# Kernel tuning notes

Measured on AMD Instinct MI355X. Metric: run time of the kernel, lower is better.

## Reference

```python
import jax, jax.numpy as jnp
import numpy as np

B, T = 1024, 128
T_IN, A_IN, V_IN = 300, 74, 35
D = 128            # dim_capsule
H = D // 2
ROUTING = 3
LABEL = 1


def _glorot(key, shape):
    fan_out, fan_in = shape[-2], shape[-1]
    s = jnp.sqrt(2.0 / (fan_in + fan_out)).astype(jnp.float32)
    return jax.random.normal(key, shape, jnp.float32) * s


def setup_inputs() -> dict:
    k = iter(jax.random.split(jax.random.key(0), 40))
    inp = {}
    inp["text"] = jax.random.normal(next(k), (B, T, T_IN), jnp.float32)
    inp["audio"] = jax.random.normal(next(k), (B, T, A_IN), jnp.float32)
    inp["video"] = jax.random.normal(next(k), (B, T, V_IN), jnp.float32)
    # bidirectional encoder LSTMs (hidden = D//2 per direction); biases b = b_ih + b_hh
    for p, din in (("t", T_IN), ("a", A_IN), ("v", V_IN)):
        for d in ("f", "b"):
            inp[p + "_Wih_" + d] = _glorot(next(k), (4 * H, din))
            inp[p + "_Whh_" + d] = _glorot(next(k), (4 * H, H))
            inp[p + "_b_" + d] = jnp.zeros((4 * H,), jnp.float32)
    # 4 capsule projection matrices per modality, stacked [4, D, D]
    inp["Wt"] = _glorot(next(k), (4, D, D))
    inp["Wa"] = _glorot(next(k), (4, D, D))
    inp["Wv"] = _glorot(next(k), (4, D, D))
    # routing LSTMs (ta, tv, av, tav) stacked on leading axis
    inp["r_Wih"] = _glorot(next(k), (4, 4 * D, D))
    inp["r_Whh"] = _glorot(next(k), (4, 4 * D, D))
    inp["r_b"] = jnp.zeros((4, 4 * D), jnp.float32)
    # decision bidirectional LSTM (hidden = D per direction)
    for d in ("f", "b"):
        inp["d_Wih_" + d] = _glorot(next(k), (4 * D, D))
        inp["d_Whh_" + d] = _glorot(next(k), (4 * D, D))
        inp["d_b_" + d] = jnp.zeros((4 * D,), jnp.float32)
    inp["fc1_W"] = _glorot(next(k), (H, D))
    inp["fc1_b"] = jnp.zeros((H,), jnp.float32)
    inp["fc2_W"] = _glorot(next(k), (LABEL, H))
    inp["fc2_b"] = jnp.zeros((LABEL,), jnp.float32)
    inp["batch_size"] = B
    return inp


def _lstm_final(x, Wih, Whh, b):
    # x: [B, T, I] -> final hidden state [B, Hh]; torch gate order i, f, g, o
    Hh = Whh.shape[-1]
    z = jnp.zeros((x.shape[0], Hh), x.dtype)

    def step(carry, xt):
        h, c = carry
        g = xt @ Wih.T + h @ Whh.T + b
        i, f, gg, o = jnp.split(g, 4, axis=-1)
        c = jax.nn.sigmoid(f) * c + jax.nn.sigmoid(i) * jnp.tanh(gg)
        h = jax.nn.sigmoid(o) * jnp.tanh(c)
        return (h, c), None

    (h, _), _ = jax.lax.scan(step, (z, z), jnp.swapaxes(x, 0, 1))
    return h


def _forward(text, audio, video,
             t_Wih_f, t_Whh_f, t_b_f, t_Wih_b, t_Whh_b, t_b_b,
             a_Wih_f, a_Whh_f, a_b_f, a_Wih_b, a_Whh_b, a_b_b,
             v_Wih_f, v_Whh_f, v_b_f, v_Wih_b, v_Whh_b, v_b_b,
             Wt, Wa, Wv, r_Wih, r_Whh, r_b,
             d_Wih_f, d_Whh_f, d_b_f, d_Wih_b, d_Whh_b, d_b_b,
             fc1_W, fc1_b, fc2_W, fc2_b):
    Bsz = text.shape[0]

    def ctx(x, Wf, Uf, bf, Wb, Ub, bb):
        # biLSTM final hidden, fwd||bwd concat -> [B, 1, D]
        hf = _lstm_final(x, Wf, Uf, bf)
        hb = _lstm_final(x[:, ::-1], Wb, Ub, bb)
        return jnp.concatenate([hf, hb], -1)[:, None, :]

    tc = ctx(text, t_Wih_f, t_Whh_f, t_b_f, t_Wih_b, t_Whh_b, t_b_b)
    ac = ctx(audio, a_Wih_f, a_Whh_f, a_b_f, a_Wih_b, a_Whh_b, a_b_b)
    vc = ctx(video, v_Wih_f, v_Whh_f, v_b_f, v_Wih_b, v_Whh_b, v_b_b)

    tusc = jnp.einsum('bod,kde->kboe', tc, Wt)   # [4, B, 1, D]
    ausc = jnp.einsum('bod,kde->kboe', ac, Wa)
    vusc = jnp.einsum('bod,kde->kboe', vc, Wv)

    pre = [jnp.concatenate([tusc[0], ausc[0]], 1),                # ta  [B,2,D]
           jnp.concatenate([tusc[1], vusc[0]], 1),                # tv  [B,2,D]
           jnp.concatenate([ausc[1], vusc[1]], 1),                # av  [B,2,D]
           jnp.concatenate([tusc[2], ausc[2], vusc[2]], 1)]       # tav [B,3,D]

    rc = [jnp.ones((Bsz, n, D), text.dtype) for n in (2, 2, 2, 3, 7)]
    dc = None
    for r in range(ROUTING + 1):
        rc = [jax.nn.softmax(c, axis=1) for c in rc]
        # per-pair routing LSTMs, final hidden [B,1,D]
        bc = [_lstm_final(rc[i] * pre[i], r_Wih[i], r_Whh[i], r_b[i])[:, None, :]
              for i in range(4)]
        deci = jnp.concatenate([tusc[3], ausc[3], vusc[3]] + bc, 1)  # [B,7,D]
        xd = rc[4] * deci
        # decision biLSTM: sum of both directions' final hidden -> [B,1,D]
        dc = (_lstm_final(xd, d_Wih_f, d_Whh_f, d_b_f)
              + _lstm_final(xd[:, ::-1], d_Wih_b, d_Whh_b, d_b_b))[:, None, :]
        if r < ROUTING:
            # agreement update: bmm gives [B,n,1], broadcasts over last dim (== repeat)
            rc = [rc[i] + jnp.matmul(pre[i], jnp.swapaxes(bc[i], 1, 2)) for i in range(4)] \
                 + [rc[4] + jnp.matmul(deci, jnp.swapaxes(dc, 1, 2))]

    dc = dc[:, 0, :]
    o1 = jnp.tanh(dc @ fc1_W.T + fc1_b)
    return o1 @ fc2_W.T + fc2_b   # mosi: no output tanh


def reference(text, audio, video,
              t_Wih_f, t_Whh_f, t_b_f, t_Wih_b, t_Whh_b, t_b_b,
              a_Wih_f, a_Whh_f, a_b_f, a_Wih_b, a_Whh_b, a_b_b,
              v_Wih_f, v_Whh_f, v_b_f, v_Wih_b, v_Whh_b, v_b_b,
              Wt, Wa, Wv, r_Wih, r_Whh, r_b,
              d_Wih_f, d_Whh_f, d_b_f, d_Wih_b, d_Whh_b, d_b_b,
              fc1_W, fc1_b, fc2_W, fc2_b, batch_size):
    return _forward(text, audio, video,
                    t_Wih_f, t_Whh_f, t_b_f, t_Wih_b, t_Whh_b, t_b_b,
                    a_Wih_f, a_Whh_f, a_b_f, a_Wih_b, a_Whh_b, a_b_b,
                    v_Wih_f, v_Whh_f, v_b_f, v_Wih_b, v_Whh_b, v_b_b,
                    Wt, Wa, Wv, r_Wih, r_Whh, r_b,
                    d_Wih_f, d_Whh_f, d_b_f, d_Wih_b, d_Whh_b, d_b_b,
                    fc1_W, fc1_b, fc2_W, fc2_b)
```

## Files before the change

kernel.cpp:

```cpp
#include <hip/hip_runtime.h>

typedef __bf16 bf16;
typedef _Float16 f16;
typedef f16 f16x8 __attribute__((ext_vector_type(8)));
typedef float f32x4 __attribute__((ext_vector_type(4)));

__device__ __forceinline__ f32x4 mfma16h(f16x8 a, f16x8 b, f32x4 c) {
  return __builtin_amdgcn_mfma_f32_16x16x32_f16(a, b, c, 0, 0, 0);
}
__device__ __forceinline__ float sigm(float x) { return 1.0f / (1.0f + __expf(-x)); }
__device__ __forceinline__ float tanh_f(float x) {
  float e = __expf(-2.0f * fabsf(x));
  return copysignf((1.0f - e) / (1.0f + e), x);
}
__device__ __forceinline__ float ldin(const void* p, long i, int f32m) {
  if (f32m) return ((const float*)p)[i];
  unsigned u = (unsigned)((const unsigned short*)p)[i] << 16;
  return __uint_as_float(u);
}
__device__ __forceinline__ unsigned short f16u(f16 h) { return __builtin_bit_cast(unsigned short, h); }
__device__ __forceinline__ float bfc(unsigned short s) { return __uint_as_float((unsigned)s << 16); }

__global__ void detect_dtype(const unsigned short* __restrict__ p, int* __restrict__ flag) {
  __shared__ int cnt;
  if (threadIdx.x == 0) cnt = 0;
  __syncthreads();
  int c = 0;
  for (int i = threadIdx.x; i < 4096; i += 256) {
    unsigned e = (p[2 * i] >> 7) & 0xFFu;
    if (e >= 0xC0u) ++c;
  }
  atomicAdd(&cnt, c);
  __syncthreads();
  if (threadIdx.x == 0) *flag = (cnt > 64) ? 1 : 0;
}


struct PadArgs { const void* src[6]; };
struct HiloArgs { const void* src[12]; int n[12]; int off[12]; };
struct F32Args { const void* src[16]; int n[16]; int off[16]; };

__global__ void conv_all(PadArgs pa, HiloArgs ha, F32Args fa,
                         f16* __restrict__ wo, float* __restrict__ fm,
                         const int* __restrict__ flag) {
  const int y = blockIdx.y;
  const int f32m = *flag;
  if (y < 6) {
    const int dinT[6] = {300, 300, 74, 74, 35, 35};
    const int kpT[6] = {320, 320, 96, 96, 64, 64};
    const int offT[6] = {0, 81920, 163840, 188416, 212992, 229376};
    int din = dinT[y], kp = kpT[y];
    const void* s = pa.src[y];
    f16* o = wo + offT[y];
    int total = 256 * kp;
    for (int i = blockIdx.x * blockDim.x + threadIdx.x; i < total; i += gridDim.x * blockDim.x) {
      int n = i / kp, k = i - n * kp;
      float v = (k < din) ? ldin(s, n * din + k, f32m) : 0.0f;
      o[i] = (f16)v;
    }
  } else if (y < 18) {
    int j = y - 6;
    int n = ha.n[j];
    const void* s = ha.src[j];
    f16* o = wo + ha.off[j];
    for (int i = blockIdx.x * blockDim.x + threadIdx.x; i < n; i += gridDim.x * blockDim.x)
      o[i] = (f16)ldin(s, i, f32m);
  } else {
    int j = y - 18;
    int n = fa.n[j];
    const void* s = fa.src[j];
    float* d = fm + fa.off[j];
    for (int i = blockIdx.x * blockDim.x + threadIdx.x; i < n; i += gridDim.x * blockDim.x)
      d[i] = ldin(s, i, f32m);
  }
}

__global__ void init_rc(float* __restrict__ rcs) {
  int i = blockIdx.x * 256 + threadIdx.x;
  if (i < 16384) rcs[i] = 1.0f;
}

struct TriArgs {
  const void* x[3];
  const f16* wAll;
  const float* fmisc;
  float* ctx;
  const int* flag;
};

template <int DIN, int KP, int CHUNK, int F32M>
__device__ void tri_body(const void* __restrict__ xsrc,
                         const f16* __restrict__ wp, const f16* __restrict__ whh,
                         const float* __restrict__ bias, float* __restrict__ ctx,
                         int m, int d, int b0, char* sm) {
  constexpr int XP = KP + 8;
  constexpr int NKS = KP / 32;
  constexpr int NCH = DIN / CHUNK;
  constexpr int ITER = (NCH + 15) / 16;

  f16 (*Xhi)[XP] = (f16 (*)[XP])sm;
  f16 (*Xlo)[XP] = (f16 (*)[XP])(sm + 32 * XP * 2);
  f16 (*hbuf)[16][72] = (f16 (*)[16][72])(sm + 64 * XP * 2);
  float* gbuf = (float*)(sm + 64 * XP * 2 + 4608);

  const int tid = threadIdx.x;
  const int lane = tid & 63, n16 = lane & 15, q = lane >> 4, w8 = tid >> 6;
  const int srow = tid & 31, sct = tid >> 5;
  const int hc = tid & 63, rr = tid >> 6;

  f16x8 wihr[2][NKS];
  f16x8 whr[2][2];
#pragma unroll
  for (int t = 0; t < 2; ++t) {
    int cc = (w8 + t * 8) * 16 + n16;
#pragma unroll
    for (int ks = 0; ks < NKS; ++ks)
      wihr[t][ks] = *(const f16x8*)(wp + cc * KP + ks * 32 + q * 8);
#pragma unroll
    for (int ks = 0; ks < 2; ++ks)
      whr[t][ks] = *(const f16x8*)(whh + cc * 64 + ks * 32 + q * 8);
  }
  float bgm[4];
#pragma unroll
  for (int g = 0; g < 4; ++g) bgm[g] = bias[g * 64 + hc];

  {
    unsigned* z = (unsigned*)sm;
    int nz = (64 * XP * 2 + 4608) >> 2;
    for (int i = tid; i < nz; i += 512) z[i] = 0u;
  }

  uint4 pf[ITER];
  auto stage_load = [&](int tg) {
#pragma unroll
    for (int i = 0; i < ITER; ++i) {
      int c = sct + i * 16;
      if (c < NCH) {
        int tl = srow >> 4, bb = srow & 15;
        int t = tg * 2 + tl; if (d) t = 127 - t;
        long base = ((long)(b0 + bb) * 128 + t) * DIN + c * CHUNK;
        if (F32M) {
          const float* p = (const float*)xsrc + base;
          if constexpr (CHUNK == 4) pf[i] = *(const uint4*)p;
          else if constexpr (CHUNK == 2) { uint2 v = *(const uint2*)p; pf[i].x = v.x; pf[i].y = v.y; }
          else pf[i].x = *(const unsigned*)p;
        } else {
          const unsigned short* p = (const unsigned short*)xsrc + base;
          if constexpr (CHUNK == 4) { uint2 v = *(const uint2*)p; pf[i].x = v.x; pf[i].y = v.y; }
          else if constexpr (CHUNK == 2) pf[i].x = *(const unsigned*)p;
          else pf[i].x = *p;
        }
      }
    }
  };
  auto stage_store = [&]() {
#pragma unroll
    for (int i = 0; i < ITER; ++i) {
      int c = sct + i * 16;
      if (c < NCH) {
        float v[4];
        if (F32M) {
          v[0] = __uint_as_float(pf[i].x); v[1] = __uint_as_float(pf[i].y);
          v[2] = __uint_as_float(pf[i].z); v[3] = __uint_as_float(pf[i].w);
        } else {
          v[0] = bfc((unsigned short)(pf[i].x & 0xFFFF));
          v[1] = bfc((unsigned short)(pf[i].x >> 16));
          v[2] = bfc((unsigned short)(pf[i].y & 0xFFFF));
          v[3] = bfc((unsigned short)(pf[i].y >> 16));
        }
        unsigned short hb[4], lb[4];
#pragma unroll
        for (int e = 0; e < CHUNK; ++e) {
          f16 h = (f16)v[e];
          hb[e] = f16u(h);
          lb[e] = f16u((f16)(v[e] - (float)h));
        }
        if constexpr (CHUNK == 4) {
          uint2 H; H.x = hb[0] | ((unsigned)hb[1] << 16); H.y = hb[2] | ((unsigned)hb[3] << 16);
          *(uint2*)&Xhi[srow][c * 4] = H;
          if (F32M) {
            uint2 L; L.x = lb[0] | ((unsigned)lb[1] << 16); L.y = lb[2] | ((unsigned)lb[3] << 16);
            *(uint2*)&Xlo[srow][c * 4] = L;
          }
        } else if constexpr (CHUNK == 2) {
          *(unsigned*)&Xhi[srow][c * 2] = hb[0] | ((unsigned)hb[1] << 16);
          if (F32M) *(unsigned*)&Xlo[srow][c * 2] = lb[0] | ((unsigned)lb[1] << 16);
        } else {
          *(unsigned short*)&Xhi[srow][c] = hb[0];
          if (F32M) *(unsigned short*)&Xlo[srow][c] = lb[0];
        }
      }
    }
  };

  float c2[2] = {0.f, 0.f};
  stage_load(0);
  __syncthreads();

  for (int tg = 0; tg < 64; ++tg) {
    stage_store();
    if (tg < 63) stage_load(tg + 1);
    __syncthreads();

    f32x4 a00, a01, a10, a11;
    {
      const f32x4 zf = {0.f, 0.f, 0.f, 0.f};
      a00 = zf; a01 = zf; a10 = zf; a11 = zf;
    }
#pragma unroll
    for (int ks = 0; ks < NKS; ++ks) {
      f16x8 ah0 = *(const f16x8*)(&Xhi[n16][ks * 32 + q * 8]);
      f16x8 ah1 = *(const f16x8*)(&Xhi[16 + n16][ks * 32 + q * 8]);
      a00 = mfma16h(ah0, wihr[0][ks], a00);
      a01 = mfma16h(ah0, wihr[1][ks], a01);
      a10 = mfma16h(ah1, wihr[0][ks], a10);
      a11 = mfma16h(ah1, wihr[1][ks], a11);
      if (F32M) {
        f16x8 al0 = *(const f16x8*)(&Xlo[n16][ks * 32 + q * 8]);
        f16x8 al1 = *(const f16x8*)(&Xlo[16 + n16][ks * 32 + q * 8]);
        a00 = mfma16h(al0, wihr[0][ks], a00);
        a01 = mfma16h(al0, wihr[1][ks], a01);
        a10 = mfma16h(al1, wihr[0][ks], a10);
        a11 = mfma16h(al1, wihr[1][ks], a11);
      }
    }

    {
      f16x8 h0 = *(const f16x8*)(&hbuf[0][n16][q * 8]);
      f16x8 h1 = *(const f16x8*)(&hbuf[0][n16][32 + q * 8]);
      a00 = mfma16h(h0, whr[0][0], a00); a00 = mfma16h(h1, whr[0][1], a00);
      a01 = mfma16h(h0, whr[1][0], a01); a01 = mfma16h(h1, whr[1][1], a01);
    }
#pragma unroll
    for (int e = 0; e < 4; ++e) {
      gbuf[(q * 4 + e) * 260 + w8 * 16 + n16] = a00[e];
      gbuf[(q * 4 + e) * 260 + 128 + w8 * 16 + n16] = a01[e];
    }
    __syncthreads();

#pragma unroll
    for (int e = 0; e < 2; ++e) {
      int row = rr + e * 8;
      float gi = gbuf[row * 260 + hc] + bgm[0];
      float gf = gbuf[row * 260 + 64 + hc] + bgm[1];
      float gg = gbuf[row * 260 + 128 + hc] + bgm[2];
      float go = gbuf[row * 260 + 192 + hc] + bgm[3];
      float c = sigm(gf) * c2[e] + sigm(gi) * tanh_f(gg);
      c2[e] = c;
      float h = sigm(go) * tanh_f(c);
      hbuf[1][row][hc] = (f16)h;
    }
    __syncthreads();

    {
      f16x8 h0 = *(const f16x8*)(&hbuf[1][n16][q * 8]);
      f16x8 h1 = *(const f16x8*)(&hbuf[1][n16][32 + q * 8]);
      a10 = mfma16h(h0, whr[0][0], a10); a10 = mfma16h(h1, whr[0][1], a10);
      a11 = mfma16h(h0, whr[1][0], a11); a11 = mfma16h(h1, whr[1][1], a11);
    }
#pragma unroll
    for (int e = 0; e < 4; ++e) {
      gbuf[(q * 4 + e) * 260 + w8 * 16 + n16] = a10[e];
      gbuf[(q * 4 + e) * 260 + 128 + w8 * 16 + n16] = a11[e];
    }
    __syncthreads();

    const bool lastStep = (tg == 63);
#pragma unroll
    for (int e = 0; e < 2; ++e) {
      int row = rr + e * 8;
      float gi = gbuf[row * 260 + hc] + bgm[0];
      float gf = gbuf[row * 260 + 64 + hc] + bgm[1];
      float gg = gbuf[row * 260 + 128 + hc] + bgm[2];
      float go = gbuf[row * 260 + 192 + hc] + bgm[3];
      float c = sigm(gf) * c2[e] + sigm(gi) * tanh_f(gg);
      c2[e] = c;
      float h = sigm(go) * tanh_f(c);
      hbuf[0][row][hc] = (f16)h;
      if (lastStep) ctx[(m * 1024 + b0 + row) * 128 + d * 64 + hc] = h;
    }
  }
}

__global__ __launch_bounds__(512, 2) void tri_lstm(TriArgs A) {
  __shared__ __align__(16) char sm[64 * 328 * 2 + 4608 + 16640];
  int bid = blockIdx.x;
  int md = bid >> 6, xb = bid & 63;
  int m = md >> 1, d = md & 1, b0 = xb * 16;
  const int wpOffT[6] = {0, 81920, 163840, 188416, 212992, 229376};
  const f16* wp = A.wAll + wpOffT[md];
  const f16* whh = A.wAll + 245760 + md * 16384;
  const float* bias = A.fmisc + md * 256;
  int f32m = *A.flag;
  if (f32m) {
    if (m == 0)      tri_body<300, 320, 4, 1>(A.x[0], wp, whh, bias, A.ctx, m, d, b0, sm);
    else if (m == 1) tri_body<74, 96, 2, 1>(A.x[1], wp, whh, bias, A.ctx, m, d, b0, sm);
    else             tri_body<35, 64, 1, 1>(A.x[2], wp, whh, bias, A.ctx, m, d, b0, sm);
  } else {
    if (m == 0)      tri_body<300, 320, 4, 0>(A.x[0], wp, whh, bias, A.ctx, m, d, b0, sm);
    else if (m == 1) tri_body<74, 96, 2, 0>(A.x[1], wp, whh, bias, A.ctx, m, d, b0, sm);
    else             tri_body<35, 64, 1, 0>(A.x[2], wp, whh, bias, A.ctx, m, d, b0, sm);
  }
}

__global__ __launch_bounds__(128) void usc_kern(const float* __restrict__ ctx,
                                                const float* __restrict__ fmisc,
                                                float* __restrict__ usc) {
  __shared__ float cr[4][128];
  int b0 = blockIdx.x * 4;
  int mk = blockIdx.y, mod = mk >> 2;
  int e = threadIdx.x;
  const float* W = fmisc + 4608 + mk * 16384;
  for (int i = e; i < 512; i += 128) {
    int r = i >> 7, dd = i & 127;
    cr[r][dd] = ctx[(mod * 1024 + b0 + r) * 128 + dd];
  }
  __syncthreads();
  float a0 = 0.f, a1 = 0.f, a2 = 0.f, a3 = 0.f;
  for (int dd = 0; dd < 128; ++dd) {
    float wv = W[dd * 128 + e];
    a0 += cr[0][dd] * wv; a1 += cr[1][dd] * wv;
    a2 += cr[2][dd] * wv; a3 += cr[3][dd] * wv;
  }
  usc[(mk * 1024 + b0 + 0) * 128 + e] = a0;
  usc[(mk * 1024 + b0 + 1) * 128 + e] = a1;
  usc[(mk * 1024 + b0 + 2) * 128 + e] = a2;
  usc[(mk * 1024 + b0 + 3) * 128 + e] = a3;
}

#define LSTM_STEP_DECL \
  const int tid = threadIdx.x; \
  const int lane = tid & 63, n16 = lane & 15, q = lane >> 4, w = tid >> 6; \
  const int u = w * 16 + n16; \
  const int u2 = tid & 127, rgg = tid >> 7;

__device__ __forceinline__ void lstm_step_mfma_r(
    f32x4* acc, const f16 (*xh)[16][136], const f16 (*xl)[16][136],
    const f16 (*hh)[16][136], int p,
    const f16x8 (*bhf)[4], const f16x8 (*whf)[4],
    int n16, int q) {
#pragma unroll
  for (int ks = 0; ks < 4; ++ks) {
    f16x8 axh = *(const f16x8*)(&xh[p][n16][ks * 32 + q * 8]);
    f16x8 axl = *(const f16x8*)(&xl[p][n16][ks * 32 + q * 8]);
    f16x8 ahh = *(const f16x8*)(&hh[p][n16][ks * 32 + q * 8]);
#pragma unroll
    for (int g = 0; g < 4; ++g) {
      acc[g] = mfma16h(axh, bhf[g][ks], acc[g]);
      acc[g] = mfma16h(axl, bhf[g][ks], acc[g]);
      acc[g] = mfma16h(ahh, whf[g][ks], acc[g]);
    }
  }
}

__global__ __launch_bounds__(512) void rchain(const float* __restrict__ usc,
                                              const float* __restrict__ rcs,
                                              const f16* __restrict__ wAll,
                                              const float* __restrict__ fmisc,
                                              float* __restrict__ bcg) {
  __shared__ __align__(16) f16 xh[2][16][136], xl[2][16][136], hh[2][16][136];
  __shared__ float rcl[16][3];
  LSTM_STEP_DECL
  const int chain = blockIdx.y;
  const int b0 = blockIdx.x * 16;
  const int WihOff[4] = {344064, 409600, 475136, 540672};
  const int WhhOff[4] = {606208, 671744, 737280, 802816};
  const int bOff[4] = {1536, 2048, 2560, 3072};
  const int ns = (chain == 3) ? 3 : 2;

  if (tid < 16) {
    int row = tid;
    int goff = (chain == 3) ? 6 : chain * 2;
    float v[3], mx = -1e30f;
    for (int j = 0; j < ns; ++j) { v[j] = rcs[(b0 + row) * 16 + goff + j]; mx = fmaxf(mx, v[j]); }
    float s = 0.f;
    for (int j = 0; j < ns; ++j) { v[j] = __expf(v[j] - mx); s += v[j]; }
    float inv = 1.0f / s;
    for (int j = 0; j < ns; ++j) rcl[row][j] = v[j] * inv;
  }
  for (int i = tid; i < 2 * 16 * 136; i += 512) (&hh[0][0][0])[i] = (f16)0.0f;

  const f16* Whh = wAll + WhhOff[chain];
  const f16* Wih = wAll + WihOff[chain];
  f16x8 whf[4][4], bhf[4][4];
#pragma unroll
  for (int g = 0; g < 4; ++g)
#pragma unroll
    for (int ks = 0; ks < 4; ++ks) {
      whf[g][ks] = *(const f16x8*)(Whh + (g * 128 + u) * 128 + ks * 32 + q * 8);
      bhf[g][ks] = *(const f16x8*)(Wih + (g * 128 + u) * 128 + ks * 32 + q * 8);
    }
  const float* bias = fmisc + bOff[chain];
  float bg[4];
#pragma unroll
  for (int g = 0; g < 4; ++g) bg[g] = bias[g * 128 + u];

  const int preMk0[4] = {0, 1, 5, 2};
  const int preMk1[4] = {4, 8, 9, 6};
  float creg[4] = {0.f, 0.f, 0.f, 0.f};

  float pv[4];
  {
    int mk0 = preMk0[chain];
#pragma unroll
    for (int rr = 0; rr < 4; ++rr)
      pv[rr] = usc[(mk0 * 1024 + b0 + rgg * 4 + rr) * 128 + u2];
  }
  __syncthreads();

  for (int s = 0; s < ns; ++s) {
    int p = s & 1;
#pragma unroll
    for (int rr = 0; rr < 4; ++rr) {
      int row = rgg * 4 + rr;
      float xv = rcl[row][s] * pv[rr];
      f16 xhv = (f16)xv;
      xh[p][row][u2] = xhv;
      xl[p][row][u2] = (f16)(xv - (float)xhv);
    }
    if (s + 1 < ns) {
      int mk2 = (s + 1 == 1) ? preMk1[chain] : 10;
#pragma unroll
      for (int rr = 0; rr < 4; ++rr)
        pv[rr] = usc[(mk2 * 1024 + b0 + rgg * 4 + rr) * 128 + u2];
    }
    __syncthreads();
    f32x4 acc[4];
    const f32x4 zf = {0.f, 0.f, 0.f, 0.f};
#pragma unroll
    for (int g = 0; g < 4; ++g) acc[g] = zf;
    lstm_step_mfma_r(acc, xh, xl, hh, p, bhf, whf, n16, q);
#pragma unroll
    for (int e = 0; e < 4; ++e) {
      int row = q * 4 + e;
      float gi = acc[0][e] + bg[0];
      float gf = acc[1][e] + bg[1];
      float gg = acc[2][e] + bg[2];
      float go = acc[3][e] + bg[3];
      float c = sigm(gf) * creg[e] + sigm(gi) * tanh_f(gg);
      creg[e] = c;
      float h = sigm(go) * tanh_f(c);
      hh[p ^ 1][row][u] = (f16)h;
      if (s == ns - 1) bcg[(chain * 1024 + b0 + row) * 128 + u] = h;
    }
  }
}

__global__ __launch_bounds__(512) void decision(const float* __restrict__ usc,
                                                const float* __restrict__ rcs,
                                                const f16* __restrict__ wAll,
                                                const float* __restrict__ fmisc,
                                                const float* __restrict__ bcg,
                                                float* __restrict__ dcF,
                                                float* __restrict__ dcB) {
  __shared__ __align__(16) f16 xh[2][16][136], xl[2][16][136], hh[2][16][136];
  __shared__ float rcl[16][7];
  LSTM_STEP_DECL
  const int dir = blockIdx.y;
  const int b0 = blockIdx.x * 16;

  if (tid < 16) {
    int row = tid;
    float v[7], mx = -1e30f;
    for (int j = 0; j < 7; ++j) { v[j] = rcs[(b0 + row) * 16 + 9 + j]; mx = fmaxf(mx, v[j]); }
    float s = 0.f;
    for (int j = 0; j < 7; ++j) { v[j] = __expf(v[j] - mx); s += v[j]; }
    float inv = 1.0f / s;
    for (int j = 0; j < 7; ++j) rcl[row][j] = v[j] * inv;
  }
  for (int i = tid; i < 2 * 16 * 136; i += 512) (&hh[0][0][0])[i] = (f16)0.0f;

  const int WihOffD[2] = {868352, 999424};
  const int WhhOffD[2] = {933888, 1064960};
  const int bOffD[2] = {3584, 4096};
  const f16* Whh = wAll + WhhOffD[dir];
  const f16* Wih = wAll + WihOffD[dir];
  f16x8 whf[4][4], bhf[4][4];
#pragma unroll
  for (int g = 0; g < 4; ++g)
#pragma unroll
    for (int ks = 0; ks < 4; ++ks) {
      whf[g][ks] = *(const f16x8*)(Whh + (g * 128 + u) * 128 + ks * 32 + q * 8);
      bhf[g][ks] = *(const f16x8*)(Wih + (g * 128 + u) * 128 + ks * 32 + q * 8);
    }
  const float* bias = fmisc + bOffD[dir];
  float bg[4];
#pragma unroll
  for (int g = 0; g < 4; ++g) bg[g] = bias[g * 128 + u];

  const int dmk[3] = {3, 7, 11};
  float creg[4] = {0.f, 0.f, 0.f, 0.f};

  float pv[4];
  {
    int j0 = dir ? 6 : 0;
#pragma unroll
    for (int rr = 0; rr < 4; ++rr) {
      int row = rgg * 4 + rr;
      pv[rr] = (j0 < 3) ? usc[(dmk[j0] * 1024 + b0 + row) * 128 + u2]
                        : bcg[((j0 - 3) * 1024 + b0 + row) * 128 + u2];
    }
  }
  __syncthreads();

  for (int s = 0; s < 7; ++s) {
    int p = s & 1;
    int j = dir ? (6 - s) : s;
#pragma unroll
    for (int rr = 0; rr < 4; ++rr) {
      int row = rgg * 4 + rr;
      float xv = rcl[row][j] * pv[rr];
      f16 xhv = (f16)xv;
      xh[p][row][u2] = xhv;
      xl[p][row][u2] = (f16)(xv - (float)xhv);
    }
    if (s < 6) {
      int j2 = dir ? (5 - s) : (s + 1);
#pragma unroll
      for (int rr = 0; rr < 4; ++rr) {
        int row = rgg * 4 + rr;
        pv[rr] = (j2 < 3) ? usc[(dmk[j2] * 1024 + b0 + row) * 128 + u2]
                          : bcg[((j2 - 3) * 1024 + b0 + row) * 128 + u2];
      }
    }
    __syncthreads();
    f32x4 acc[4];
    const f32x4 zf = {0.f, 0.f, 0.f, 0.f};
#pragma unroll
    for (int g = 0; g < 4; ++g) acc[g] = zf;
    lstm_step_mfma_r(acc, xh, xl, hh, p, bhf, whf, n16, q);
#pragma unroll
    for (int e = 0; e < 4; ++e) {
      int row = q * 4 + e;
      float gi = acc[0][e] + bg[0];
      float gf = acc[1][e] + bg[1];
      float gg = acc[2][e] + bg[2];
      float go = acc[3][e] + bg[3];
      float c = sigm(gf) * creg[e] + sigm(gi) * tanh_f(gg);
      creg[e] = c;
      float h = sigm(go) * tanh_f(c);
      hh[p ^ 1][row][u] = (f16)h;
      if (s == 6) {
        if (dir == 0) dcF[(b0 + row) * 128 + u] = h;
        else dcB[(b0 + row) * 128 + u] = h;
      }
    }
  }
}

__global__ __launch_bounds__(256) void rupdate(const float* __restrict__ usc,
                                               const float* __restrict__ bcg,
                                               const float* __restrict__ dcF,
                                               const float* __restrict__ dcB,
                                               float* __restrict__ rcs,
                                               float* __restrict__ dcw, int last) {
  __shared__ float dsum[16][128];
  __shared__ float rcl[16][16];
  const int tid = threadIdx.x;
  const int b0 = blockIdx.x * 16;
  for (int i = tid; i < 2048; i += 256) {
    int row = i >> 7, col = i & 127;
    float v = dcF[(b0 + row) * 128 + col] + dcB[(b0 + row) * 128 + col];
    dsum[row][col] = v;
    if (last) dcw[(b0 + row) * 128 + col] = v;
  }
  {
    int row = tid >> 4, cap = tid & 15;
    rcl[row][cap] = rcs[(b0 + row) * 16 + cap];
  }
  __syncthreads();
  if (!last) {
    int row = tid >> 4, cap = tid & 15;
    const int goffT[16] = {0, 0, 2, 2, 4, 4, 6, 6, 6, 9, 9, 9, 9, 9, 9, 9};
    const int gnT[16] = {2, 2, 2, 2, 2, 2, 3, 3, 3, 7, 7, 7, 7, 7, 7, 7};
    int go = goffT[cap], gn = gnT[cap];
    float mx = -1e30f;
    for (int j = 0; j < gn; ++j) mx = fmaxf(mx, rcl[row][go + j]);
    float s = 0.f;
    for (int j = 0; j < gn; ++j) s += __expf(rcl[row][go + j] - mx);
    float sm = __expf(rcl[row][cap] - mx) / s;

    const int preMkTab[9] = {0, 4, 1, 8, 5, 9, 2, 6, 10};
    float a = 0.f;
    if (cap < 9) {
      int i = (cap < 6) ? (cap >> 1) : 3;
      const float* pr = usc + (preMkTab[cap] * 1024 + b0 + row) * 128;
      const float* bcrow = bcg + (i * 1024 + b0 + row) * 128;
      for (int dd = 0; dd < 128; ++dd) a += pr[dd] * bcrow[dd];
    } else {
      int j = cap - 9;
      if (j < 3) {
        const int dmk[3] = {3, 7, 11};
        const float* pr = usc + (dmk[j] * 1024 + b0 + row) * 128;
        for (int dd = 0; dd < 128; ++dd) a += pr[dd] * dsum[row][dd];
      } else {
        const float* bcrow = bcg + ((j - 3) * 1024 + b0 + row) * 128;
        for (int dd = 0; dd < 128; ++dd) a += bcrow[dd] * dsum[row][dd];
      }
    }
    rcs[(b0 + row) * 16 + cap] = sm + a;
  }
}

__global__ __launch_bounds__(64) void head(const float* __restrict__ dc, const float* __restrict__ fcw,
                                           void* __restrict__ out, const int* __restrict__ flag) {
  int b = blockIdx.x, j = threadIdx.x;
  const float* r = dc + b * 128;
  float acc = fcw[209408 + j];
  for (int dd = 0; dd < 128; ++dd) acc += r[dd] * fcw[201216 + j * 128 + dd];
  float o = tanh_f(acc) * fcw[209472 + j];
  for (int off = 32; off; off >>= 1) o += __shfl_down(o, off, 64);
  if (j == 0) {
    float res = o + fcw[209536];
    if (*flag) ((float*)out)[b] = res;
    else ((bf16*)out)[b] = (bf16)res;
  }
}

extern "C" void kernel_launch(void* const* d_in, const int* in_sizes, int n_in,
                              void* d_out, int out_size, void* d_ws, size_t ws_size,
                              hipStream_t stream) {
  float* fw = (float*)d_ws;
  int* flag = (int*)d_ws;
  float* ctx = fw + 4;
  float* usc = ctx + 393216;
  float* dcw = usc + 1572864;
  float* fmisc = dcw + 131072;
  float* rcs = fmisc + 209552;
  float* bcg = rcs + 16384;
  float* dcF = bcg + 524288;
  float* dcB = dcF + 131072;
  f16* wAll = (f16*)(dcB + 131072);

  hipLaunchKernelGGL(detect_dtype, dim3(1), dim3(256), 0, stream,
                     (const unsigned short*)d_in[0], flag);

  PadArgs pa;
  HiloArgs ha;
  for (int m = 0; m < 3; ++m)
    for (int dd = 0; dd < 2; ++dd) {
      int md = m * 6 + dd * 3;
      pa.src[m * 2 + dd] = d_in[3 + md + 0];
      ha.src[m * 2 + dd] = d_in[3 + md + 1];
      ha.n[m * 2 + dd] = 16384;
      ha.off[m * 2 + dd] = 245760 + (m * 2 + dd) * 16384;
    }
  const int hsrc[6] = {24, 25, 27, 28, 30, 31};
  const int hn[6] = {262144, 262144, 65536, 65536, 65536, 65536};
  const int hoff[6] = {344064, 606208, 868352, 933888, 999424, 1064960};
  for (int j = 0; j < 6; ++j) { ha.src[6 + j] = d_in[hsrc[j]]; ha.n[6 + j] = hn[j]; ha.off[6 + j] = hoff[j]; }

  F32Args fa;
  for (int m = 0; m < 3; ++m)
    for (int dd = 0; dd < 2; ++dd) {
      fa.src[m * 2 + dd] = d_in[3 + m * 6 + dd * 3 + 2];
      fa.n[m * 2 + dd] = 256;
      fa.off[m * 2 + dd] = (m * 2 + dd) * 256;
    }
  const int fsrc[10] = {26, 29, 32, 21, 22, 23, 33, 34, 35, 36};
  const int fn[10] = {2048, 512, 512, 65536, 65536, 65536, 8192, 64, 64, 1};
  const int foff[10] = {1536, 3584, 4096, 4608, 70144, 135680, 201216, 209408, 209472, 209536};
  for (int j = 0; j < 10; ++j) { fa.src[6 + j] = d_in[fsrc[j]]; fa.n[6 + j] = fn[j]; fa.off[6 + j] = foff[j]; }

  hipLaunchKernelGGL(conv_all, dim3(64, 34), dim3(256), 0, stream,
                     pa, ha, fa, wAll, fmisc, (const int*)flag);
  hipLaunchKernelGGL(init_rc, dim3(64), dim3(256), 0, stream, rcs);

  TriArgs ta;
  ta.x[0] = d_in[0]; ta.x[1] = d_in[1]; ta.x[2] = d_in[2];
  ta.wAll = wAll; ta.fmisc = fmisc; ta.ctx = ctx; ta.flag = flag;
  hipLaunchKernelGGL(tri_lstm, dim3(384), dim3(512), 0, stream, ta);

  hipLaunchKernelGGL(usc_kern, dim3(256, 12), dim3(128), 0, stream,
                     (const float*)ctx, (const float*)fmisc, usc);

  for (int r = 0; r < 4; ++r) {
    hipLaunchKernelGGL(rchain, dim3(64, 4), dim3(512), 0, stream,
                       (const float*)usc, (const float*)rcs, (const f16*)wAll,
                       (const float*)fmisc, bcg);
    hipLaunchKernelGGL(decision, dim3(64, 2), dim3(512), 0, stream,
                       (const float*)usc, (const float*)rcs, (const f16*)wAll,
                       (const float*)fmisc, (const float*)bcg, dcF, dcB);
    hipLaunchKernelGGL(rupdate, dim3(64), dim3(256), 0, stream,
                       (const float*)usc, (const float*)bcg, (const float*)dcF,
                       (const float*)dcB, rcs, dcw, (r == 3) ? 1 : 0);
  }

  hipLaunchKernelGGL(head, dim3(1024), dim3(64), 0, stream,
                     (const float*)dcw, (const float*)fmisc, d_out, (const int*)flag);
}
```

Measured before the change: 803.6 us.

## Fuse routing-coefficient update into rchain/decision prologues and double-buffer state

```diff
diff --git a/kernel.cpp b/kernel.cpp
--- a/kernel.cpp
+++ b/kernel.cpp
@@ -34,7 +34,6 @@
   __syncthreads();
   if (threadIdx.x == 0) *flag = (cnt > 64) ? 1 : 0;
 }
-
 
 struct PadArgs { const void* src[6]; };
 struct HiloArgs { const void* src[12]; int n[12]; int off[12]; };
@@ -73,11 +72,6 @@
     for (int i = blockIdx.x * blockDim.x + threadIdx.x; i < n; i += gridDim.x * blockDim.x)
       d[i] = ldin(s, i, f32m);
   }
-}
-
-__global__ void init_rc(float* __restrict__ rcs) {
-  int i = blockIdx.x * 256 + threadIdx.x;
-  if (i < 16384) rcs[i] = 1.0f;
 }
 
 struct TriArgs {
@@ -334,6 +328,49 @@
   const int u = w * 16 + n16; \
   const int u2 = tid & 127, rgg = tid >> 7;
 
+#define RCS_PROLOGUE(ROWS, DEST) \
+  if (tid < (ROWS) * 16) { \
+    int prow = tid >> 4, cap = tid & 15; \
+    float v = 1.0f; \
+    if (r > 0) { \
+      const int goffT[16] = {0, 0, 2, 2, 4, 4, 6, 6, 6, 9, 9, 9, 9, 9, 9, 9}; \
+      const int gnT[16] = {2, 2, 2, 2, 2, 2, 3, 3, 3, 7, 7, 7, 7, 7, 7, 7}; \
+      const int preMkTab[9] = {0, 4, 1, 8, 5, 9, 2, 6, 10}; \
+      const int dmkT[3] = {3, 7, 11}; \
+      int gn = gnT[cap]; \
+      float smv; \
+      if (r == 1) smv = 1.0f / (float)gn; \
+      else { \
+        int go = goffT[cap]; \
+        float mx = -1e30f; \
+        for (int j2 = 0; j2 < gn; ++j2) mx = fmaxf(mx, rcsIn[(b0 + prow) * 16 + go + j2]); \
+        float ssum = 0.f; \
+        for (int j2 = 0; j2 < gn; ++j2) ssum += __expf(rcsIn[(b0 + prow) * 16 + go + j2] - mx); \
+        smv = __expf(rcsIn[(b0 + prow) * 16 + cap] - mx) / ssum; \
+      } \
+      float a = 0.f; \
+      if (cap < 9) { \
+        int ii = (cap < 6) ? (cap >> 1) : 3; \
+        const float* pr = usc + (preMkTab[cap] * 1024 + b0 + prow) * 128; \
+        const float* bcrow = bcgPrev + (ii * 1024 + b0 + prow) * 128; \
+        for (int dd = 0; dd < 128; ++dd) a += pr[dd] * bcrow[dd]; \
+      } else { \
+        int j2 = cap - 9; \
+        const float* df = dcFprev + (b0 + prow) * 128; \
+        const float* db2 = dcBprev + (b0 + prow) * 128; \
+        if (j2 < 3) { \
+          const float* pr = usc + (dmkT[j2] * 1024 + b0 + prow) * 128; \
+          for (int dd = 0; dd < 128; ++dd) a += pr[dd] * (df[dd] + db2[dd]); \
+        } else { \
+          const float* bcrow = bcgPrev + ((j2 - 3) * 1024 + b0 + prow) * 128; \
+          for (int dd = 0; dd < 128; ++dd) a += bcrow[dd] * (df[dd] + db2[dd]); \
+        } \
+      } \
+      v = smv + a; \
+    } \
+    (DEST)[prow][cap] = v; \
+  }
+
 __device__ __forceinline__ void lstm_step_mfma_r(
     f32x4* acc, const f16 (*xh)[16][136], const f16 (*xl)[16][136],
     const f16 (*hh)[16][136], int p,
@@ -354,11 +391,17 @@
 }
 
 __global__ __launch_bounds__(512) void rchain(const float* __restrict__ usc,
-                                              const float* __restrict__ rcs,
+                                              const float* __restrict__ rcsIn,
+                                              float* __restrict__ rcsOut,
                                               const f16* __restrict__ wAll,
                                               const float* __restrict__ fmisc,
-                                              float* __restrict__ bcg) {
+                                              const float* __restrict__ bcgPrev,
+                                              const float* __restrict__ dcFprev,
+                                              const float* __restrict__ dcBprev,
+                                              float* __restrict__ bcg,
+                                              int r) {
   __shared__ __align__(16) f16 xh[2][16][136], xl[2][16][136], hh[2][16][136];
+  __shared__ float rr16[16][16];
   __shared__ float rcl[16][3];
   LSTM_STEP_DECL
   const int chain = blockIdx.y;
@@ -368,17 +411,21 @@
   const int bOff[4] = {1536, 2048, 2560, 3072};
   const int ns = (chain == 3) ? 3 : 2;
 
+  RCS_PROLOGUE(16, rr16)
+  for (int i = tid; i < 2 * 16 * 136; i += 512) (&hh[0][0][0])[i] = (f16)0.0f;
+  __syncthreads();
   if (tid < 16) {
     int row = tid;
     int goff = (chain == 3) ? 6 : chain * 2;
     float v[3], mx = -1e30f;
-    for (int j = 0; j < ns; ++j) { v[j] = rcs[(b0 + row) * 16 + goff + j]; mx = fmaxf(mx, v[j]); }
+    for (int j = 0; j < ns; ++j) { v[j] = rr16[row][goff + j]; mx = fmaxf(mx, v[j]); }
     float s = 0.f;
     for (int j = 0; j < ns; ++j) { v[j] = __expf(v[j] - mx); s += v[j]; }
     float inv = 1.0f / s;
     for (int j = 0; j < ns; ++j) rcl[row][j] = v[j] * inv;
   }
-  for (int i = tid; i < 2 * 16 * 136; i += 512) (&hh[0][0][0])[i] = (f16)0.0f;
+  if (chain == 0 && (r == 1 || r == 2) && tid < 256)
+    rcsOut[(b0 + (tid >> 4)) * 16 + (tid & 15)] = rr16[tid >> 4][tid & 15];
 
   const f16* Whh = wAll + WhhOff[chain];
   const f16* Wih = wAll + WihOff[chain];
@@ -403,17 +450,17 @@
   {
     int mk0 = preMk0[chain];
 #pragma unroll
-    for (int rr = 0; rr < 4; ++rr)
-      pv[rr] = usc[(mk0 * 1024 + b0 + rgg * 4 + rr) * 128 + u2];
+    for (int rr2 = 0; rr2 < 4; ++rr2)
+      pv[rr2] = usc[(mk0 * 1024 + b0 + rgg * 4 + rr2) * 128 + u2];
   }
   __syncthreads();
 
   for (int s = 0; s < ns; ++s) {
     int p = s & 1;
 #pragma unroll
-    for (int rr = 0; rr < 4; ++rr) {
-      int row = rgg * 4 + rr;
-      float xv = rcl[row][s] * pv[rr];
+    for (int rr2 = 0; rr2 < 4; ++rr2) {
+      int row = rgg * 4 + rr2;
+      float xv = rcl[row][s] * pv[rr2];
       f16 xhv = (f16)xv;
       xh[p][row][u2] = xhv;
       xl[p][row][u2] = (f16)(xv - (float)xhv);
@@ -421,8 +468,8 @@
     if (s + 1 < ns) {
       int mk2 = (s + 1 == 1) ? preMk1[chain] : 10;
 #pragma unroll
-      for (int rr = 0; rr < 4; ++rr)
-        pv[rr] = usc[(mk2 * 1024 + b0 + rgg * 4 + rr) * 128 + u2];
+      for (int rr2 = 0; rr2 < 4; ++rr2)
+        pv[rr2] = usc[(mk2 * 1024 + b0 + rgg * 4 + rr2) * 128 + u2];
     }
     __syncthreads();
     f32x4 acc[4];
@@ -447,28 +494,39 @@
 }
 
 __global__ __launch_bounds__(512) void decision(const float* __restrict__ usc,
-                                                const float* __restrict__ rcs,
+                                                const float* __restrict__ rcsIn,
                                                 const f16* __restrict__ wAll,
                                                 const float* __restrict__ fmisc,
+                                                const float* __restrict__ bcgPrev,
+                                                const float* __restrict__ dcFprev,
+                                                const float* __restrict__ dcBprev,
                                                 const float* __restrict__ bcg,
                                                 float* __restrict__ dcF,
-                                                float* __restrict__ dcB) {
+                                                float* __restrict__ dcB,
+                                                int r) {
   __shared__ __align__(16) f16 xh[2][16][136], xl[2][16][136], hh[2][16][136];
-  __shared__ float rcl[16][7];
+  __shared__ float rr16[8][16];
+  __shared__ float rcl[8][7];
   LSTM_STEP_DECL
   const int dir = blockIdx.y;
-  const int b0 = blockIdx.x * 16;
-
-  if (tid < 16) {
+  const int b0 = blockIdx.x * 8;
+
+  for (int i = tid; i < 2 * 16 * 136; i += 512) {
+    (&xh[0][0][0])[i] = (f16)0.0f;
+    (&xl[0][0][0])[i] = (f16)0.0f;
+    (&hh[0][0][0])[i] = (f16)0.0f;
+  }
+  RCS_PROLOGUE(8, rr16)
+  __syncthreads();
+  if (tid < 8) {
     int row = tid;
     float v[7], mx = -1e30f;
-    for (int j = 0; j < 7; ++j) { v[j] = rcs[(b0 + row) * 16 + 9 + j]; mx = fmaxf(mx, v[j]); }
+    for (int j = 0; j < 7; ++j) { v[j] = rr16[row][9 + j]; mx = fmaxf(mx, v[j]); }
     float s = 0.f;
     for (int j = 0; j < 7; ++j) { v[j] = __expf(v[j] - mx); s += v[j]; }
     float inv = 1.0f / s;
     for (int j = 0; j < 7; ++j) rcl[row][j] = v[j] * inv;
   }
-  for (int i = tid; i < 2 * 16 * 136; i += 512) (&hh[0][0][0])[i] = (f16)0.0f;
 
   const int WihOffD[2] = {868352, 999424};
   const int WhhOffD[2] = {933888, 1064960};
@@ -491,14 +549,14 @@
   const int dmk[3] = {3, 7, 11};
   float creg[4] = {0.f, 0.f, 0.f, 0.f};
 
-  float pv[4];
+  float pv[2];
   {
     int j0 = dir ? 6 : 0;
 #pragma unroll
-    for (int rr = 0; rr < 4; ++rr) {
-      int row = rgg * 4 + rr;
-      pv[rr] = (j0 < 3) ? usc[(dmk[j0] * 1024 + b0 + row) * 128 + u2]
-                        : bcg[((j0 - 3) * 1024 + b0 + row) * 128 + u2];
+    for (int rr2 = 0; rr2 < 2; ++rr2) {
+      int row = rgg * 2 + rr2;
+      pv[rr2] = (j0 < 3) ? usc[(dmk[j0] * 1024 + b0 + row) * 128 + u2]
+                         : bcg[((j0 - 3) * 1024 + b0 + row) * 128 + u2];
     }
   }
   __syncthreads();
@@ -507,9 +565,9 @@
     int p = s & 1;
     int j = dir ? (6 - s) : s;
 #pragma unroll
-    for (int rr = 0; rr < 4; ++rr) {
-      int row = rgg * 4 + rr;
-      float xv = rcl[row][j] * pv[rr];
+    for (int rr2 = 0; rr2 < 2; ++rr2) {
+      int row = rgg * 2 + rr2;
+      float xv = rcl[row][j] * pv[rr2];
       f16 xhv = (f16)xv;
       xh[p][row][u2] = xhv;
       xl[p][row][u2] = (f16)(xv - (float)xhv);
@@ -517,10 +575,10 @@
     if (s < 6) {
       int j2 = dir ? (5 - s) : (s + 1);
 #pragma unroll
-      for (int rr = 0; rr < 4; ++rr) {
-        int row = rgg * 4 + rr;
-        pv[rr] = (j2 < 3) ? usc[(dmk[j2] * 1024 + b0 + row) * 128 + u2]
-                          : bcg[((j2 - 3) * 1024 + b0 + row) * 128 + u2];
+      for (int rr2 = 0; rr2 < 2; ++rr2) {
+        int row = rgg * 2 + rr2;
+        pv[rr2] = (j2 < 3) ? usc[(dmk[j2] * 1024 + b0 + row) * 128 + u2]
+                           : bcg[((j2 - 3) * 1024 + b0 + row) * 128 + u2];
       }
     }
     __syncthreads();
@@ -540,7 +598,7 @@
       creg[e] = c;
       float h = sigm(go) * tanh_f(c);
       hh[p ^ 1][row][u] = (f16)h;
-      if (s == 6) {
+      if (s == 6 && row < 8) {
         if (dir == 0) dcF[(b0 + row) * 128 + u] = h;
         else dcB[(b0 + row) * 128 + u] = h;
       }
@@ -548,66 +606,15 @@
   }
 }
 
-__global__ __launch_bounds__(256) void rupdate(const float* __restrict__ usc,
-                                               const float* __restrict__ bcg,
-                                               const float* __restrict__ dcF,
-                                               const float* __restrict__ dcB,
-                                               float* __restrict__ rcs,
-                                               float* __restrict__ dcw, int last) {
-  __shared__ float dsum[16][128];
-  __shared__ float rcl[16][16];
-  const int tid = threadIdx.x;
-  const int b0 = blockIdx.x * 16;
-  for (int i = tid; i < 2048; i += 256) {
-    int row = i >> 7, col = i & 127;
-    float v = dcF[(b0 + row) * 128 + col] + dcB[(b0 + row) * 128 + col];
-    dsum[row][col] = v;
-    if (last) dcw[(b0 + row) * 128 + col] = v;
-  }
-  {
-    int row = tid >> 4, cap = tid & 15;
-    rcl[row][cap] = rcs[(b0 + row) * 16 + cap];
-  }
-  __syncthreads();
-  if (!last) {
-    int row = tid >> 4, cap = tid & 15;
-    const int goffT[16] = {0, 0, 2, 2, 4, 4, 6, 6, 6, 9, 9, 9, 9, 9, 9, 9};
-    const int gnT[16] = {2, 2, 2, 2, 2, 2, 3, 3, 3, 7, 7, 7, 7, 7, 7, 7};
-    int go = goffT[cap], gn = gnT[cap];
-    float mx = -1e30f;
-    for (int j = 0; j < gn; ++j) mx = fmaxf(mx, rcl[row][go + j]);
-    float s = 0.f;
-    for (int j = 0; j < gn; ++j) s += __expf(rcl[row][go + j] - mx);
-    float sm = __expf(rcl[row][cap] - mx) / s;
-
-    const int preMkTab[9] = {0, 4, 1, 8, 5, 9, 2, 6, 10};
-    float a = 0.f;
-    if (cap < 9) {
-      int i = (cap < 6) ? (cap >> 1) : 3;
-      const float* pr = usc + (preMkTab[cap] * 1024 + b0 + row) * 128;
-      const float* bcrow = bcg + (i * 1024 + b0 + row) * 128;
-      for (int dd = 0; dd < 128; ++dd) a += pr[dd] * bcrow[dd];
-    } else {
-      int j = cap - 9;
-      if (j < 3) {
-        const int dmk[3] = {3, 7, 11};
-        const float* pr = usc + (dmk[j] * 1024 + b0 + row) * 128;
-        for (int dd = 0; dd < 128; ++dd) a += pr[dd] * dsum[row][dd];
-      } else {
-        const float* bcrow = bcg + ((j - 3) * 1024 + b0 + row) * 128;
-        for (int dd = 0; dd < 128; ++dd) a += bcrow[dd] * dsum[row][dd];
-      }
-    }
-    rcs[(b0 + row) * 16 + cap] = sm + a;
-  }
-}
-
-__global__ __launch_bounds__(64) void head(const float* __restrict__ dc, const float* __restrict__ fcw,
+__global__ __launch_bounds__(64) void head(const float* __restrict__ dcFl,
+                                           const float* __restrict__ dcBl,
+                                           const float* __restrict__ fcw,
                                            void* __restrict__ out, const int* __restrict__ flag) {
   int b = blockIdx.x, j = threadIdx.x;
-  const float* r = dc + b * 128;
+  const float* rf = dcFl + b * 128;
+  const float* rb = dcBl + b * 128;
   float acc = fcw[209408 + j];
-  for (int dd = 0; dd < 128; ++dd) acc += r[dd] * fcw[201216 + j * 128 + dd];
+  for (int dd = 0; dd < 128; ++dd) acc += (rf[dd] + rb[dd]) * fcw[201216 + j * 128 + dd];
   float o = tanh_f(acc) * fcw[209472 + j];
   for (int off = 32; off; off >>= 1) o += __shfl_down(o, off, 64);
   if (j == 0) {
@@ -624,13 +631,16 @@
   int* flag = (int*)d_ws;
   float* ctx = fw + 4;
   float* usc = ctx + 393216;
-  float* dcw = usc + 1572864;
-  float* fmisc = dcw + 131072;
-  float* rcs = fmisc + 209552;
-  float* bcg = rcs + 16384;
-  float* dcF = bcg + 524288;
-  float* dcB = dcF + 131072;
-  f16* wAll = (f16*)(dcB + 131072);
+  float* fmisc = usc + 1572864;
+  float* bcg0 = fmisc + 209552;
+  float* bcg1 = bcg0 + 524288;
+  float* dcF0 = bcg1 + 524288;
+  float* dcF1 = dcF0 + 131072;
+  float* dcB0 = dcF1 + 131072;
+  float* dcB1 = dcB0 + 131072;
+  float* rcsA = dcB1 + 131072;
+  float* rcsB = rcsA + 16384;
+  f16* wAll = (f16*)(rcsB + 16384);
 
   hipLaunchKernelGGL(detect_dtype, dim3(1), dim3(256), 0, stream,
                      (const unsigned short*)d_in[0], flag);
@@ -664,7 +674,6 @@
 
   hipLaunchKernelGGL(conv_all, dim3(64, 34), dim3(256), 0, stream,
                      pa, ha, fa, wAll, fmisc, (const int*)flag);
-  hipLaunchKernelGGL(init_rc, dim3(64), dim3(256), 0, stream, rcs);
 
   TriArgs ta;
   ta.x[0] = d_in[0]; ta.x[1] = d_in[1]; ta.x[2] = d_in[2];
@@ -674,18 +683,26 @@
   hipLaunchKernelGGL(usc_kern, dim3(256, 12), dim3(128), 0, stream,
                      (const float*)ctx, (const float*)fmisc, usc);
 
+  float* bcgP[2] = {bcg0, bcg1};
+  float* dcFP[2] = {dcF0, dcF1};
+  float* dcBP[2] = {dcB0, dcB1};
   for (int r = 0; r < 4; ++r) {
+    int cp = r & 1, pp = cp ^ 1;
+    const float* rcsIn = (r == 3) ? rcsB : rcsA;
+    float* rcsOut = (r == 2) ? rcsB : rcsA;
     hipLaunchKernelGGL(rchain, dim3(64, 4), dim3(512), 0, stream,
-                       (const float*)usc, (const float*)rcs, (const f16*)wAll,
-                       (const float*)fmisc, bcg);
-    hipLaunchKernelGGL(decision, dim3(64, 2), dim3(512), 0, stream,
-                       (const float*)usc, (const float*)rcs, (const f16*)wAll,
-                       (const float*)fmisc, (const float*)bcg, dcF, dcB);
-    hipLaunchKernelGGL(rupdate, dim3(64), dim3(256), 0, stream,
-                       (const float*)usc, (const float*)bcg, (const float*)dcF,
-                       (const float*)dcB, rcs, dcw, (r == 3) ? 1 : 0);
+                       (const float*)usc, rcsIn, rcsOut, (const f16*)wAll,
+                       (const float*)fmisc, (const float*)bcgP[pp],
+                       (const float*)dcFP[pp], (const float*)dcBP[pp],
+                       bcgP[cp], r);
+    hipLaunchKernelGGL(decision, dim3(128, 2), dim3(512), 0, stream,
+                       (const float*)usc, rcsIn, (const f16*)wAll,
+                       (const float*)fmisc, (const float*)bcgP[pp],
+                       (const float*)dcFP[pp], (const float*)dcBP[pp],
+                       (const float*)bcgP[cp], dcFP[cp], dcBP[cp], r);
   }
 
   hipLaunchKernelGGL(head, dim3(1024), dim3(64), 0, stream,
-                     (const float*)dcw, (const float*)fmisc, d_out, (const int*)flag);
-}
+                     (const float*)dcF1, (const float*)dcB1, (const float*)fmisc,
+                     d_out, (const int*)flag);
+}
```

New measurement: 834.5 us. 1.04x slower.
